# Kernel tuning notes

Hardware: AMD Instinct MI355X
Metric: run time of the kernel (lower is better)

Reference implementation:

```python
import jax, jax.numpy as jnp
import numpy as np
from jax import lax

EPS = 1e-8

def _conv(x, w, b):
    # x: [B,Cin,H,W], w: [Cout,Cin,kh,kw] (torch OIHW layout), SAME padding, stride 1
    y = lax.conv_general_dilated(x, w, (1, 1), 'SAME',
                                 dimension_numbers=('NCHW', 'OIHW', 'NCHW'))
    return y + b[None, :, None, None]

def setup_inputs() -> dict:
    key = jax.random.key(0)
    ks = jax.random.split(key, 16)
    B, S, H, A, NZ, NO = 256, 4, 32, 5, 150, 17
    d = {
        'map_in': jax.random.uniform(ks[0], (B, 2, H, H), jnp.float32),
        'b0': jax.random.uniform(ks[1], (B, H, H), jnp.float32),
        'act_in': jax.random.randint(ks[2], (B, S), 0, A),
        'obs_in': jax.random.uniform(ks[3], (B, S, 4), jnp.float32),
        'is_start': 1,
        'step_size': S,
        'VI_k': 64,
        # parameters, initialized per the torch init scheme
        'Tb_w': 1.0 / 9.0 + jax.random.normal(ks[4], (A, 1, 3, 3)) / 90.0,
        'Tb_b': jnp.zeros((A,)),
        'Tv_w': 1.0 / 9.0 + jax.random.normal(ks[5], (A, 1, 3, 3)) / 90.0,
        'Tv_b': jnp.zeros((A,)),
        'Z1_w': jax.random.normal(ks[6], (NZ, 1, 3, 3)) / 3.0,
        'Z1_b': jnp.zeros((NZ,)),
        'Z2_w': jax.random.normal(ks[7], (NO, NZ, 1, 1)) / np.sqrt(NZ),
        'Z2_b': jnp.zeros((NO,)),
        'O1_w': jax.random.normal(ks[8], (NO, 4)) * 0.25,
        'O1_b': jnp.zeros((NO,)),
        'O3_w': jax.random.normal(ks[9], (NO, NO)) / NO,
        'O3_b': jnp.zeros((NO,)),
        'R1_w': jax.random.normal(ks[10], (NZ, 2, 3, 3)) / np.sqrt(18.0),
        'R1_b': jnp.zeros((NZ,)),
        'R2_w': jax.random.normal(ks[11], (A, NZ, 1, 1)) / np.sqrt(NZ),
        'R2_b': jnp.zeros((A,)),
        'FL_w': jax.random.normal(ks[12], (A, A)) * 0.25,
        'FL_b': jnp.zeros((A,)),
    }
    return d

def reference(map_in, b0, act_in, obs_in, is_start, step_size, VI_k,
              Tb_w, Tb_b, Tv_w, Tv_b, Z1_w, Z1_b, Z2_w, Z2_b,
              O1_w, O1_b, O3_w, O3_b, R1_w, R1_b, R2_w, R2_b, FL_w, FL_b):
    B, _, H, W = map_in.shape
    A = Tb_w.shape[0]

    # ---- VI: value iteration conv+add+max loop ----
    R = _conv(jax.nn.relu(_conv(map_in, R1_w, R1_b)), R2_w, R2_b)  # [B,A,H,W]
    v0 = jnp.zeros((B, 1, H, W), map_in.dtype)
    Q0 = jnp.zeros_like(R)

    def vi_step(carry, _):
        v, _Q = carry
        Q = _conv(v, Tv_w, Tv_b) + R
        v = jnp.max(Q, axis=1, keepdims=True)
        return (v, Q), None

    (_, Q), _ = lax.scan(vi_step, (v0, Q0), None, length=VI_k)
    Q = jnp.transpose(Q, (0, 2, 3, 1))  # [B,H,W,A]

    # ---- observation model Z ----
    Z = jax.nn.sigmoid(_conv(_conv(map_in[:, :1], Z1_w, Z1_b), Z2_w, Z2_b))
    Z = jnp.transpose(Z, (0, 2, 3, 1))  # [B,H,W,17]
    Z = Z / (jnp.sum(Z, axis=3, keepdims=True) + EPS)

    # ---- recurrent Bayes filter + policy ----
    b = b0 if is_start else b0  # is_start resets belief to b0 (always true here)
    outs = []
    for t in range(step_size):  # small fixed recurrence length
        o = obs_in[:, t]  # [B,4]
        w = jax.nn.softmax(jnp.tanh(o @ O1_w.T + O1_b) @ O3_w.T + O3_b, axis=1)  # [B,17]
        Z_O = jnp.einsum('bhwo,bo->bhw', Z, w)
        bp = jnp.transpose(_conv(b[:, None], Tb_w, Tb_b), (0, 2, 3, 1))  # [B,H,W,A]
        a1h = jax.nn.one_hot(act_in[:, t], A, dtype=bp.dtype)
        b_pa = jnp.einsum('bhwa,ba->bhw', bp, a1h)
        b_next = b_pa * Z_O
        b = b_next / (jnp.sum(b_next, axis=(1, 2), keepdims=True) + EPS)
        Qb = jnp.einsum('bhwa,bhw->ba', Q, b)
        outs.append(Qb @ FL_w.T + FL_b)
    outputs = jnp.concatenate(outs, axis=0)  # [step_size*B, A]
    return outputs, b
```

## Files before the change

### kernel.cpp

```cpp
#include <hip/hip_runtime.h>

#define EPSV 1e-8f
#define PW   34
#define NPIX 1024
#define NA   5
#define NOUT 17
#define NZC  150

__global__ __launch_bounds__(1024) void vin_fused(
    const float* __restrict__ map_in, const float* __restrict__ b0,
    const int*   __restrict__ act_in, const float* __restrict__ obs_in,
    const int*   __restrict__ step_p, const int*   __restrict__ vik_p,
    const float* __restrict__ Tb_w,  const float* __restrict__ Tb_b,
    const float* __restrict__ Tv_w,  const float* __restrict__ Tv_b,
    const float* __restrict__ Z1_w,  const float* __restrict__ Z1_b,
    const float* __restrict__ Z2_w,  const float* __restrict__ Z2_b,
    const float* __restrict__ O1_w,  const float* __restrict__ O1_b,
    const float* __restrict__ O3_w,  const float* __restrict__ O3_b,
    const float* __restrict__ R1_w,  const float* __restrict__ R1_b,
    const float* __restrict__ R2_w,  const float* __restrict__ R2_b,
    const float* __restrict__ FL_w,  const float* __restrict__ FL_b,
    float* __restrict__ out, int B)
{
    __shared__ float map0[PW*PW], map1[PW*PW], v_lds[PW*PW], b_lds[PW*PW];
    __shared__ float zc_w[NOUT*9], zc_b[NOUT];
    __shared__ float h_lds[NOUT], u_lds[NOUT], w_lds[NOUT];
    __shared__ float partials[16][6], sums[6];

    const int tid  = threadIdx.x;
    const int blk  = blockIdx.x;
    const int y    = tid >> 5, x = tid & 31;
    const int pidx = (y + 1) * PW + (x + 1);
    const int lane = tid & 63, wvid = tid >> 6;

    for (int i = tid; i < PW*PW; i += NPIX) {
        map0[i] = 0.f; map1[i] = 0.f; v_lds[i] = 0.f; b_lds[i] = 0.f;
    }
    __syncthreads();
    map0[pidx]  = map_in[blk*2*NPIX + tid];
    map1[pidx]  = map_in[blk*2*NPIX + NPIX + tid];
    b_lds[pidx] = b0[blk*NPIX + tid];

    if (tid < NOUT*9) {
        const int o = tid / 9, k = tid % 9;
        float s = 0.f;
        for (int c = 0; c < NZC; ++c) s += Z2_w[o*NZC + c] * Z1_w[c*9 + k];
        zc_w[tid] = s;
    } else if (tid < NOUT*9 + NOUT) {
        const int o = tid - NOUT*9;
        float s = Z2_b[o];
        for (int c = 0; c < NZC; ++c) s += Z2_w[o*NZC + c] * Z1_b[c];
        zc_b[o] = s;
    }
    __syncthreads();

    float m0[9], m1[9];
    #pragma unroll
    for (int k = 0; k < 9; ++k) {
        const int off = (y + k/3)*PW + x + (k%3);
        m0[k] = map0[off]; m1[k] = map1[off];
    }

    float r[NA];
    #pragma unroll
    for (int a = 0; a < NA; ++a) r[a] = R2_b[a];
    for (int c = 0; c < NZC; ++c) {
        float s = R1_b[c];
        const float* w1 = R1_w + c*18;
        #pragma unroll
        for (int k = 0; k < 9; ++k) s += m0[k] * w1[k];
        #pragma unroll
        for (int k = 0; k < 9; ++k) s += m1[k] * w1[9 + k];
        s = fmaxf(s, 0.f);
        #pragma unroll
        for (int a = 0; a < NA; ++a) r[a] += R2_w[a*NZC + c] * s;
    }

    float z[NOUT];
    float zs = 0.f;
    #pragma unroll
    for (int o = 0; o < NOUT; ++o) {
        float s = zc_b[o];
        #pragma unroll
        for (int k = 0; k < 9; ++k) s += m0[k] * zc_w[o*9 + k];
        const float zz = 1.f / (1.f + expf(-s));
        z[o] = zz; zs += zz;
    }
    const float zn = 1.f / (zs + EPSV);
    #pragma unroll
    for (int o = 0; o < NOUT; ++o) z[o] *= zn;

    float q[NA];
    #pragma unroll
    for (int a = 0; a < NA; ++a) q[a] = 0.f;
    const int K = vik_p[0];
    for (int it = 0; it < K; ++it) {
        float n[9];
        #pragma unroll
        for (int k = 0; k < 9; ++k) n[k] = v_lds[(y + k/3)*PW + x + (k%3)];
        float vmax = -3.4e38f;
        #pragma unroll
        for (int a = 0; a < NA; ++a) {
            float s = Tv_b[a] + r[a];
            #pragma unroll
            for (int k = 0; k < 9; ++k) s += n[k] * Tv_w[a*9 + k];
            q[a] = s;
            vmax = fmaxf(vmax, s);
        }
        __syncthreads();
        v_lds[pidx] = vmax;
        __syncthreads();
    }

    const int S = step_p[0];
    for (int t = 0; t < S; ++t) {
        if (tid < NOUT) {
            const float* ob = obs_in + (blk*S + t)*4;
            float hh = O1_b[tid];
            #pragma unroll
            for (int k = 0; k < 4; ++k) hh += ob[k] * O1_w[tid*4 + k];
            h_lds[tid] = tanhf(hh);
        }
        __syncthreads();
        if (tid < NOUT) {
            float u = O3_b[tid];
            for (int j = 0; j < NOUT; ++j) u += h_lds[j] * O3_w[tid*NOUT + j];
            u_lds[tid] = u;
        }
        __syncthreads();
        if (tid < NOUT) {
            float mx = u_lds[0];
            for (int j = 1; j < NOUT; ++j) mx = fmaxf(mx, u_lds[j]);
            float sm = 0.f;
            for (int j = 0; j < NOUT; ++j) sm += expf(u_lds[j] - mx);
            w_lds[tid] = expf(u_lds[tid] - mx) / sm;
        }
        __syncthreads();

        const int a_t = act_in[blk*S + t];
        float bp = Tb_b[a_t];
        #pragma unroll
        for (int k = 0; k < 9; ++k)
            bp += b_lds[(y + k/3)*PW + x + (k%3)] * Tb_w[a_t*9 + k];

        float zo = 0.f;
        #pragma unroll
        for (int o = 0; o < NOUT; ++o) zo += z[o] * w_lds[o];
        const float bn = bp * zo;

        float v6[6];
        v6[5] = bn;
        #pragma unroll
        for (int a = 0; a < NA; ++a) v6[a] = q[a] * bn;
        #pragma unroll
        for (int k = 0; k < 6; ++k) {
            float vv = v6[k];
            for (int off = 32; off > 0; off >>= 1) vv += __shfl_down(vv, off);
            v6[k] = vv;
        }
        if (lane == 0) {
            #pragma unroll
            for (int k = 0; k < 6; ++k) partials[wvid][k] = v6[k];
        }
        __syncthreads();
        if (tid < 6) {
            float s = 0.f;
            for (int w2 = 0; w2 < 16; ++w2) s += partials[w2][tid];
            sums[tid] = s;
        }
        __syncthreads();

        const float inv = 1.f / (sums[5] + EPSV);
        if (tid < NA) {
            float oj = FL_b[tid];
            #pragma unroll
            for (int a = 0; a < NA; ++a) oj += (sums[a] * inv) * FL_w[tid*NA + a];
            out[(t*B + blk)*NA + tid] = oj;
        }
        b_lds[pidx] = bn * inv;
        __syncthreads();
    }

    out[S*B*NA + blk*NPIX + tid] = b_lds[pidx];
}

extern "C" void kernel_launch(void* const* d_in, const int* in_sizes, int n_in,
                              void* d_out, int out_size, void* d_ws, size_t ws_size,
                              hipStream_t stream)
{
    const float* map_in = (const float*)d_in[0];
    const float* b0     = (const float*)d_in[1];
    const int*   act_in = (const int*)  d_in[2];
    const float* obs_in = (const float*)d_in[3];
    const int*   step_p = (const int*)  d_in[5];
    const int*   vik_p  = (const int*)  d_in[6];
    const float* Tb_w = (const float*)d_in[7];
    const float* Tb_b = (const float*)d_in[8];
    const float* Tv_w = (const float*)d_in[9];
    const float* Tv_b = (const float*)d_in[10];
    const float* Z1_w = (const float*)d_in[11];
    const float* Z1_b = (const float*)d_in[12];
    const float* Z2_w = (const float*)d_in[13];
    const float* Z2_b = (const float*)d_in[14];
    const float* O1_w = (const float*)d_in[15];
    const float* O1_b = (const float*)d_in[16];
    const float* O3_w = (const float*)d_in[17];
    const float* O3_b = (const float*)d_in[18];
    const float* R1_w = (const float*)d_in[19];
    const float* R1_b = (const float*)d_in[20];
    const float* R2_w = (const float*)d_in[21];
    const float* R2_b = (const float*)d_in[22];
    const float* FL_w = (const float*)d_in[23];
    const float* FL_b = (const float*)d_in[24];

    const int B = in_sizes[1] / NPIX;

    hipLaunchKernelGGL(vin_fused, dim3(B), dim3(1024), 0, stream,
        map_in, b0, act_in, obs_in, step_p, vik_p,
        Tb_w, Tb_b, Tv_w, Tv_b, Z1_w, Z1_b, Z2_w, Z2_b,
        O1_w, O1_b, O3_w, O3_b, R1_w, R1_b, R2_w, R2_b,
        FL_w, FL_b, (float*)d_out, B);
}
```

Before: 216.4 us.

## Precompute observation weights and Z_O upfront in LDS, freeing registers

Moves the per-step observation MLP and softmax for all steps ahead of the VI loop, computed in parallel by threads 256 and up. The per-pixel 17-entry Z vector is reduced to one Z_O value per step and stored in a new LDS buffer, so z[] no longer stays live in registers through the VI loop. Launch bounds now request 4 blocks per CU. This removes serial barriers from the filter loop and lowers register pressure, but adds 32KB of LDS per block, which may cap occupancy, and assumes at most 8 steps.

```diff
diff --git a/kernel.cpp b/kernel.cpp
--- a/kernel.cpp
+++ b/kernel.cpp
@@ -6,8 +6,9 @@
 #define NA   5
 #define NOUT 17
 #define NZC  150
-
-__global__ __launch_bounds__(1024) void vin_fused(
+#define MAXS 8
+
+__global__ __launch_bounds__(1024, 4) void vin_fused(
     const float* __restrict__ map_in, const float* __restrict__ b0,
     const int*   __restrict__ act_in, const float* __restrict__ obs_in,
     const int*   __restrict__ step_p, const int*   __restrict__ vik_p,
@@ -24,7 +25,8 @@
 {
     __shared__ float map0[PW*PW], map1[PW*PW], v_lds[PW*PW], b_lds[PW*PW];
     __shared__ float zc_w[NOUT*9], zc_b[NOUT];
-    __shared__ float h_lds[NOUT], u_lds[NOUT], w_lds[NOUT];
+    __shared__ float h_all[MAXS][NOUT], u_all[MAXS][NOUT], w_all[MAXS][NOUT];
+    __shared__ float zo_lds[MAXS * NPIX];
     __shared__ float partials[16][6], sums[6];
 
     const int tid  = threadIdx.x;
@@ -32,6 +34,9 @@
     const int y    = tid >> 5, x = tid & 31;
     const int pidx = (y + 1) * PW + (x + 1);
     const int lane = tid & 63, wvid = tid >> 6;
+
+    const int S = step_p[0];
+    const int K = vik_p[0];
 
     for (int i = tid; i < PW*PW; i += NPIX) {
         map0[i] = 0.f; map1[i] = 0.f; v_lds[i] = 0.f; b_lds[i] = 0.f;
@@ -52,6 +57,33 @@
         for (int c = 0; c < NZC; ++c) s += Z2_w[o*NZC + c] * Z1_b[c];
         zc_b[o] = s;
     }
+
+    const int mt = tid - 256;
+    const int mT = mt / NOUT, mO = mt % NOUT;
+    if (mt >= 0 && mt < S*NOUT) {
+        const float* ob = obs_in + (blk*S + mT)*4;
+        float hh = O1_b[mO];
+        #pragma unroll
+        for (int k = 0; k < 4; ++k) hh += ob[k] * O1_w[mO*4 + k];
+        h_all[mT][mO] = tanhf(hh);
+    }
+    __syncthreads();
+    if (mt >= 0 && mt < S*NOUT) {
+        float u = O3_b[mO];
+        #pragma unroll
+        for (int j = 0; j < NOUT; ++j) u += h_all[mT][j] * O3_w[mO*NOUT + j];
+        u_all[mT][mO] = u;
+    }
+    __syncthreads();
+    if (mt >= 0 && mt < S*NOUT) {
+        float mx = u_all[mT][0];
+        #pragma unroll
+        for (int j = 1; j < NOUT; ++j) mx = fmaxf(mx, u_all[mT][j]);
+        float sm = 0.f;
+        #pragma unroll
+        for (int j = 0; j < NOUT; ++j) sm += expf(u_all[mT][j] - mx);
+        w_all[mT][mO] = expf(u_all[mT][mO] - mx) / sm;
+    }
     __syncthreads();
 
     float m0[9], m1[9];
@@ -76,24 +108,29 @@
         for (int a = 0; a < NA; ++a) r[a] += R2_w[a*NZC + c] * s;
     }
 
-    float z[NOUT];
-    float zs = 0.f;
-    #pragma unroll
-    for (int o = 0; o < NOUT; ++o) {
-        float s = zc_b[o];
-        #pragma unroll
-        for (int k = 0; k < 9; ++k) s += m0[k] * zc_w[o*9 + k];
-        const float zz = 1.f / (1.f + expf(-s));
-        z[o] = zz; zs += zz;
-    }
-    const float zn = 1.f / (zs + EPSV);
-    #pragma unroll
-    for (int o = 0; o < NOUT; ++o) z[o] *= zn;
+    {
+        float z[NOUT];
+        float zs = 0.f;
+        #pragma unroll
+        for (int o = 0; o < NOUT; ++o) {
+            float s = zc_b[o];
+            #pragma unroll
+            for (int k = 0; k < 9; ++k) s += m0[k] * zc_w[o*9 + k];
+            const float zz = 1.f / (1.f + expf(-s));
+            z[o] = zz; zs += zz;
+        }
+        const float zn = 1.f / (zs + EPSV);
+        for (int t = 0; t < S; ++t) {
+            float zo = 0.f;
+            #pragma unroll
+            for (int o = 0; o < NOUT; ++o) zo += z[o] * w_all[t][o];
+            zo_lds[t*NPIX + tid] = zo * zn;
+        }
+    }
 
     float q[NA];
     #pragma unroll
     for (int a = 0; a < NA; ++a) q[a] = 0.f;
-    const int K = vik_p[0];
     for (int it = 0; it < K; ++it) {
         float n[9];
         #pragma unroll
@@ -112,41 +149,14 @@
         __syncthreads();
     }
 
-    const int S = step_p[0];
     for (int t = 0; t < S; ++t) {
-        if (tid < NOUT) {
-            const float* ob = obs_in + (blk*S + t)*4;
-            float hh = O1_b[tid];
-            #pragma unroll
-            for (int k = 0; k < 4; ++k) hh += ob[k] * O1_w[tid*4 + k];
-            h_lds[tid] = tanhf(hh);
-        }
-        __syncthreads();
-        if (tid < NOUT) {
-            float u = O3_b[tid];
-            for (int j = 0; j < NOUT; ++j) u += h_lds[j] * O3_w[tid*NOUT + j];
-            u_lds[tid] = u;
-        }
-        __syncthreads();
-        if (tid < NOUT) {
-            float mx = u_lds[0];
-            for (int j = 1; j < NOUT; ++j) mx = fmaxf(mx, u_lds[j]);
-            float sm = 0.f;
-            for (int j = 0; j < NOUT; ++j) sm += expf(u_lds[j] - mx);
-            w_lds[tid] = expf(u_lds[tid] - mx) / sm;
-        }
-        __syncthreads();
-
         const int a_t = act_in[blk*S + t];
         float bp = Tb_b[a_t];
         #pragma unroll
         for (int k = 0; k < 9; ++k)
             bp += b_lds[(y + k/3)*PW + x + (k%3)] * Tb_w[a_t*9 + k];
 
-        float zo = 0.f;
-        #pragma unroll
-        for (int o = 0; o < NOUT; ++o) zo += z[o] * w_lds[o];
-        const float bn = bp * zo;
+        const float bn = bp * zo_lds[t*NPIX + tid];
 
         float v6[6];
         v6[5] = bn;
```

After: 187.9 us. 13.1% less time.
